# Kernel optimization log

Measured on AMD Instinct MI355X. Metric: run time of the kernel, lower is better.

The kernel has to match this reference:

```python
import jax, jax.numpy as jnp
import numpy as np

D_MODEL = 768
N_HEADS = 12
D_HEAD = 64
BATCH = 4
SEQ = 2048
INIT_RANGE = 0.02
IGNORE = -1e5


def setup_inputs() -> dict:
    key = jax.random.key(0)
    ks = jax.random.split(key, 5)
    x = jax.random.normal(ks[0], (BATCH, SEQ, D_MODEL), dtype=jnp.float32)
    W_Q = jax.random.normal(ks[1], (N_HEADS, D_MODEL, D_HEAD), dtype=jnp.float32) * INIT_RANGE
    W_K = jax.random.normal(ks[2], (N_HEADS, D_MODEL, D_HEAD), dtype=jnp.float32) * INIT_RANGE
    W_V = jax.random.normal(ks[3], (N_HEADS, D_MODEL, D_HEAD), dtype=jnp.float32) * INIT_RANGE
    W_O = jax.random.normal(ks[4], (N_HEADS, D_HEAD, D_MODEL), dtype=jnp.float32) * INIT_RANGE
    b_Q = jnp.zeros((N_HEADS, D_HEAD), dtype=jnp.float32)
    b_K = jnp.zeros((N_HEADS, D_HEAD), dtype=jnp.float32)
    b_V = jnp.zeros((N_HEADS, D_HEAD), dtype=jnp.float32)
    b_O = jnp.zeros((D_MODEL,), dtype=jnp.float32)
    return {"normalized_resid_pre": x, "W_Q": W_Q, "W_K": W_K, "W_V": W_V,
            "W_O": W_O, "b_Q": b_Q, "b_K": b_K, "b_V": b_V, "b_O": b_O}


def reference(normalized_resid_pre, W_Q, W_K, W_V, W_O, b_Q, b_K, b_V, b_O):
    x = normalized_resid_pre  # [b, s, d_model]
    q = jnp.einsum('bsm,hmd->bshd', x, W_Q) + b_Q  # [b, s, h, d_head]
    k = jnp.einsum('bsm,hmd->bshd', x, W_K) + b_K
    v = jnp.einsum('bsm,hmd->bshd', x, W_V) + b_V
    scores = jnp.einsum('bqhd,bkhd->bhqk', q, k) / jnp.sqrt(jnp.float32(D_HEAD))
    seq = x.shape[1]
    causal = jnp.tril(jnp.ones((seq, seq), dtype=bool))  # True where allowed
    scores = jnp.where(causal, scores, jnp.float32(IGNORE))
    pattern = jax.nn.softmax(scores, axis=-1)  # [b, h, q, k]
    z = jnp.einsum('bhqk,bkhd->bqhd', pattern, v)
    attn_out = jnp.einsum('bqhd,hdm->bqm', z, W_O) + b_O
    return attn_out
```

## Files before the change

### kernel.cpp

```cpp
#include <hip/hip_runtime.h>
#include <math.h>

#define DEVI __device__ __forceinline__

typedef __bf16 bf16_t;
typedef bf16_t bf16x8 __attribute__((ext_vector_type(8)));
typedef float  f32x4  __attribute__((ext_vector_type(4)));

constexpr int NB   = 4;
constexpr int SEQL = 2048;
constexpr int NH   = 12;
constexpr int DHD  = 64;
constexpr int DMOD = 768;
constexpr int NT   = NB * SEQL;
constexpr int KD   = DMOD;


DEVI unsigned short f2bf(float f) {
  union { float f; unsigned u; } v; v.f = f;
  unsigned r = v.u + 0x7FFFu + ((v.u >> 16) & 1u);
  return (unsigned short)(r >> 16);
}

DEVI unsigned short cvt_bf16(float f) {
  bf16_t b = (bf16_t)f;
  return __builtin_bit_cast(unsigned short, b);
}

DEVI float exp2_raw(float x) {
  float r;
  asm("v_exp_f32 %0, %1" : "=v"(r) : "v"(x));
  return r;
}

DEVI void gload16(const unsigned short* src, unsigned short* dst) {
  auto g = (const __attribute__((address_space(1))) unsigned int*)(unsigned long long)src;
  auto l = (__attribute__((address_space(3))) unsigned int*)(unsigned int)(unsigned long long)(dst);
  __builtin_amdgcn_global_load_lds(g, l, 16, 0, 0);
}

__global__ void __launch_bounds__(256) prep_all(const float* __restrict__ x,
                                                const float* __restrict__ WQ,
                                                const float* __restrict__ WK,
                                                const float* __restrict__ WV,
                                                const float* __restrict__ WO,
                                                unsigned short* __restrict__ xb,
                                                unsigned short* __restrict__ Wt,
                                                unsigned short* __restrict__ Wo_t) {
  __shared__ float T[64][68];
  const int bid = blockIdx.x;
  const int t = threadIdx.x;
  if (bid < 3072) {
    size_t i = ((size_t)bid * 256 + t) * 8;
    float4 a = *(const float4*)(x + i);
    float4 b = *(const float4*)(x + i + 4);
    union { unsigned short u[8]; uint4 v; } pk;
    pk.u[0] = f2bf(a.x); pk.u[1] = f2bf(a.y); pk.u[2] = f2bf(a.z); pk.u[3] = f2bf(a.w);
    pk.u[4] = f2bf(b.x); pk.u[5] = f2bf(b.y); pk.u[6] = f2bf(b.z); pk.u[7] = f2bf(b.w);
    *(uint4*)(xb + i) = pk.v;
    return;
  }
  const int r0 = t >> 4, c4 = (t & 15) * 4;
  if (bid < 3504) {
    const int u = bid - 3072;
    const int mt = u % 12, hw = u / 12;
    const int which = hw / 12, h = hw % 12;
    const float* W = (which == 0) ? WQ : ((which == 1) ? WK : WV);
    const float* src = W + ((size_t)h * 768 + mt * 64) * 64;
#pragma unroll
    for (int rep = 0; rep < 4; ++rep) {
      int m = rep * 16 + r0;
      float4 v = *(const float4*)(src + m * 64 + c4);
      T[m][c4] = v.x; T[m][c4 + 1] = v.y; T[m][c4 + 2] = v.z; T[m][c4 + 3] = v.w;
    }
    __syncthreads();
    unsigned short* dst = Wt + ((size_t)which * 768 + h * 64) * 768 + mt * 64;
#pragma unroll
    for (int rep = 0; rep < 4; ++rep) {
      int d = rep * 16 + r0;
      union { unsigned short u[4]; uint2 v; } o;
#pragma unroll
      for (int j = 0; j < 4; ++j) o.u[j] = f2bf(T[c4 + j][d]);
      *(uint2*)(dst + (size_t)d * 768 + c4) = o.v;
    }
  } else {
    const int u = bid - 3504;
    const int m0 = (u % 12) * 64, hd0 = (u / 12) * 64;
#pragma unroll
    for (int rep = 0; rep < 4; ++rep) {
      int i = rep * 16 + r0;
      float4 v = *(const float4*)(WO + (size_t)(hd0 + i) * 768 + m0 + c4);
      T[i][c4] = v.x; T[i][c4 + 1] = v.y; T[i][c4 + 2] = v.z; T[i][c4 + 3] = v.w;
    }
    __syncthreads();
#pragma unroll
    for (int rep = 0; rep < 4; ++rep) {
      int m = rep * 16 + r0;
      union { unsigned short u[4]; uint2 v; } o;
#pragma unroll
      for (int j = 0; j < 4; ++j) o.u[j] = f2bf(T[c4 + j][m]);
      *(uint2*)(Wo_t + (size_t)(m0 + m) * 768 + hd0 + c4) = o.v;
    }
  }
}

__global__ void __launch_bounds__(256)
gemm_qkv(const unsigned short* __restrict__ A,
         const unsigned short* __restrict__ Bt,
         const float* __restrict__ bq, const float* __restrict__ bk,
         const float* __restrict__ bv,
         unsigned short* __restrict__ qo, unsigned short* __restrict__ ko,
         unsigned short* __restrict__ vo) {
  __shared__ __align__(16) unsigned short ldsA[2 * 8192];
  __shared__ __align__(16) unsigned short ldsB[8192];
  const int bm = blockIdx.x, bn = blockIdx.y;
  const int m0 = bm * 128, n0 = bn * 128;
  const int tid = threadIdx.x, w = tid >> 6, lane = tid & 63;
  const int g = lane >> 4, r16 = lane & 15;
  const int wm = w >> 1, wn = w & 1;

  const int ss = (lane & 7) ^ ((lane >> 3) & 7);
  const unsigned short* asrc = A  + (size_t)(m0 + (lane >> 3)) * KD + ss * 8;
  const unsigned short* bsrc = Bt + (size_t)(n0 + (lane >> 3)) * KD + ss * 8;

  auto stageA = [&](int buf, int kt) {
#pragma unroll
    for (int j = 0; j < 4; ++j) {
      int seg = w * 4 + j;
      gload16(asrc + (size_t)(seg * 8) * KD + kt * 64, ldsA + buf * 8192 + seg * 512);
    }
  };
  auto stageB = [&](int kt) {
#pragma unroll
    for (int j = 0; j < 4; ++j) {
      int seg = w * 4 + j;
      gload16(bsrc + (size_t)(seg * 8) * KD + kt * 64, ldsB + seg * 512);
    }
  };

  const int r7 = r16 & 7;
  const int aoff0 = r16 * 64 + ((g    ) ^ r7) * 8;
  const int aoff1 = r16 * 64 + ((g + 4) ^ r7) * 8;

  f32x4 acc[4][4];
  const f32x4 zero4 = {0.f, 0.f, 0.f, 0.f};
#pragma unroll
  for (int i = 0; i < 4; ++i)
#pragma unroll
    for (int j = 0; j < 4; ++j) acc[i][j] = zero4;

  constexpr int NKT = KD / 64;
  stageA(0, 0);
  stageB(0);
  int buf = 0;
  for (int kt = 0; kt < NKT; ++kt) {
    if (kt + 1 < NKT) {
      stageA(buf ^ 1, kt + 1);
      asm volatile("s_waitcnt vmcnt(4)" ::: "memory");
    } else {
      asm volatile("s_waitcnt vmcnt(0)" ::: "memory");
    }
    __builtin_amdgcn_s_barrier();
    const unsigned short* Ab = ldsA + buf * 8192 + wm * 4096;
    const unsigned short* Bb = ldsB + wn * 4096;
    bf16x8 af[2][4], bfr[2][4];
#pragma unroll
    for (int f = 0; f < 4; ++f) {
      af[0][f]  = *(const bf16x8*)&Ab[aoff0 + f * 1024];
      af[1][f]  = *(const bf16x8*)&Ab[aoff1 + f * 1024];
      bfr[0][f] = *(const bf16x8*)&Bb[aoff0 + f * 1024];
      bfr[1][f] = *(const bf16x8*)&Bb[aoff1 + f * 1024];
    }
#pragma unroll
    for (int kk = 0; kk < 2; ++kk)
#pragma unroll
      for (int fm = 0; fm < 4; ++fm)
#pragma unroll
        for (int fn = 0; fn < 4; ++fn)
          acc[fm][fn] = __builtin_amdgcn_mfma_f32_16x16x32_bf16(af[kk][fm], bfr[kk][fn],
                                                                acc[fm][fn], 0, 0, 0);
    asm volatile("s_waitcnt lgkmcnt(0)" ::: "memory");
    __builtin_amdgcn_s_barrier();
    if (kt + 1 < NKT) stageB(kt + 1);
    buf ^= 1;
  }

#pragma unroll
  for (int fm = 0; fm < 4; ++fm) {
#pragma unroll
    for (int fn = 0; fn < 4; ++fn) {
      const int col = n0 + wn * 64 + fn * 16 + r16;
      const int rbase = m0 + wm * 64 + fm * 16 + g * 4;
      const int which = (col >= 1536) ? 2 : ((col >= 768) ? 1 : 0);
      const int hd = col - which * 768;
      const int h = hd >> 6, d = hd & 63;
      const float bias = (which == 0 ? bq : which == 1 ? bk : bv)[hd];
      if (which == 2) {
        union { unsigned short u[4]; uint2 v; } o;
#pragma unroll
        for (int r = 0; r < 4; ++r) o.u[r] = cvt_bf16(acc[fm][fn][r] + bias);
        const int b = rbase >> 11, s = rbase & (SEQL - 1);
        *(uint2*)(vo + ((size_t)(b * NH + h) * DHD + d) * SEQL + s) = o.v;
      } else {
#pragma unroll
        for (int r = 0; r < 4; ++r) {
          int row = rbase + r;
          int b = row >> 11, s = row & (SEQL - 1);
          float v = acc[fm][fn][r] + bias;
          if (which == 0)
            qo[((size_t)(b * NH + h) * SEQL + s) * DHD + d] = cvt_bf16(v * 0.1803368801111f);
          else
            ko[((size_t)(b * NH + h) * SEQL + s) * DHD + d] = cvt_bf16(v);
        }
      }
    }
  }
}

__global__ void __launch_bounds__(256)
gemm_o(const unsigned short* __restrict__ A,
       const unsigned short* __restrict__ Bt,
       const float* __restrict__ bo, float* __restrict__ fout) {
  __shared__ __align__(16) unsigned short ldsA[2 * 4096];
  __shared__ __align__(16) unsigned short ldsB[8192];
  const int bm = blockIdx.x, bn = blockIdx.y;
  const int m0 = bm * 64, n0 = bn * 128;
  const int tid = threadIdx.x, w = tid >> 6, lane = tid & 63;
  const int g = lane >> 4, r16 = lane & 15;
  const int wm = w >> 1, wn = w & 1;

  const int ss = (lane & 7) ^ ((lane >> 3) & 7);
  const unsigned short* asrc = A  + (size_t)(m0 + (lane >> 3)) * KD + ss * 8;
  const unsigned short* bsrc = Bt + (size_t)(n0 + (lane >> 3)) * KD + ss * 8;

  auto stageA = [&](int buf, int kt) {
#pragma unroll
    for (int j = 0; j < 2; ++j) {
      int seg = w * 2 + j;
      gload16(asrc + (size_t)(seg * 8) * KD + kt * 64, ldsA + buf * 4096 + seg * 512);
    }
  };
  auto stageB = [&](int kt) {
#pragma unroll
    for (int j = 0; j < 4; ++j) {
      int seg = w * 4 + j;
      gload16(bsrc + (size_t)(seg * 8) * KD + kt * 64, ldsB + seg * 512);
    }
  };

  const int r7 = r16 & 7;
  const int aoff0 = r16 * 64 + ((g    ) ^ r7) * 8;
  const int aoff1 = r16 * 64 + ((g + 4) ^ r7) * 8;

  f32x4 acc[2][4];
  const f32x4 zero4 = {0.f, 0.f, 0.f, 0.f};
#pragma unroll
  for (int i = 0; i < 2; ++i)
#pragma unroll
    for (int j = 0; j < 4; ++j) acc[i][j] = zero4;

  constexpr int NKT = KD / 64;
  stageA(0, 0);
  stageB(0);
  int buf = 0;
  for (int kt = 0; kt < NKT; ++kt) {
    if (kt + 1 < NKT) {
      stageA(buf ^ 1, kt + 1);
      asm volatile("s_waitcnt vmcnt(2)" ::: "memory");
    } else {
      asm volatile("s_waitcnt vmcnt(0)" ::: "memory");
    }
    __builtin_amdgcn_s_barrier();
    const unsigned short* Ab = ldsA + buf * 4096 + wm * 2048;
    const unsigned short* Bb = ldsB + wn * 4096;
    bf16x8 af[2][2], bfr[2][4];
#pragma unroll
    for (int f = 0; f < 2; ++f) {
      af[0][f] = *(const bf16x8*)&Ab[aoff0 + f * 1024];
      af[1][f] = *(const bf16x8*)&Ab[aoff1 + f * 1024];
    }
#pragma unroll
    for (int f = 0; f < 4; ++f) {
      bfr[0][f] = *(const bf16x8*)&Bb[aoff0 + f * 1024];
      bfr[1][f] = *(const bf16x8*)&Bb[aoff1 + f * 1024];
    }
#pragma unroll
    for (int kk = 0; kk < 2; ++kk)
#pragma unroll
      for (int fm = 0; fm < 2; ++fm)
#pragma unroll
        for (int fn = 0; fn < 4; ++fn)
          acc[fm][fn] = __builtin_amdgcn_mfma_f32_16x16x32_bf16(af[kk][fm], bfr[kk][fn],
                                                                acc[fm][fn], 0, 0, 0);
    asm volatile("s_waitcnt lgkmcnt(0)" ::: "memory");
    __builtin_amdgcn_s_barrier();
    if (kt + 1 < NKT) stageB(kt + 1);
    buf ^= 1;
  }

#pragma unroll
  for (int fm = 0; fm < 2; ++fm) {
#pragma unroll
    for (int fn = 0; fn < 4; ++fn) {
      const int col = n0 + wn * 64 + fn * 16 + r16;
      const int rbase = m0 + wm * 32 + fm * 16 + g * 4;
      const float bias = bo[col];
#pragma unroll
      for (int r = 0; r < 4; ++r)
        fout[(size_t)(rbase + r) * DMOD + col] = acc[fm][fn][r] + bias;
    }
  }
}

__global__ void __launch_bounds__(256, 3)
attn_fwd(const unsigned short* __restrict__ qb,
         const unsigned short* __restrict__ kb,
         const unsigned short* __restrict__ vt,
         unsigned short* __restrict__ zb) {
  __shared__ __align__(16) unsigned short ldsK[2 * 4096];
  __shared__ __align__(16) unsigned short ldsV[2 * 4096];
  __shared__ __align__(16) unsigned short ldsP[2 * 4096];
  const int id = blockIdx.x;
  const int qp = id / 48, bh = id % 48;
  const int qtA = qp, qtB = 31 - qp;
  const int tid = threadIdx.x, w = tid >> 6, lane = tid & 63;
  const int g = lane >> 4, r16 = lane & 15;
  const int r7 = r16 & 7;

  const int sslot = (lane & 7) ^ (lane >> 3);
  const unsigned short* ksrc = kb + (size_t)bh * SEQL * DHD + (lane >> 3) * 64 + sslot * 8;
  const unsigned short* vsrc = vt + (size_t)bh * SEQL * DHD + (lane >> 3) * 2048 + sslot * 8;

  auto stage = [&](int buf, int kv0) {
#pragma unroll
    for (int j = 0; j < 2; ++j) {
      int seg = w * 2 + j;
      gload16(ksrc + kv0 * 64 + seg * 512, ldsK + buf * 4096 + seg * 512);
      gload16(vsrc + kv0 + seg * 16384,    ldsV + buf * 4096 + seg * 512);
    }
  };

  const int roff0 = r16 * 64 + ((g    ) ^ r7) * 8;
  const int roff1 = r16 * 64 + ((g + 4) ^ r7) * 8;
  char* const pwbA = (char*)ldsP + w * 2048;
  char* const pwbB = (char*)ldsP + 8192 + w * 2048;
  int paddr[4];
#pragma unroll
  for (int fn = 0; fn < 4; ++fn)
    paddr[fn] = r16 * 128 + ((((fn * 2) + (g >> 1)) ^ r7) << 4) + ((g & 1) << 3);
  const int prd0 = r16 * 128 + (((g    ) ^ r7) << 4);
  const int prd1 = r16 * 128 + (((g + 4) ^ r7) << 4);
  const int thr = w * 16 + r16 - g * 4;

  bf16x8 qfA[2], qfB[2];
  {
    const unsigned short* qa = qb + ((size_t)bh * SEQL + qtA * 64 + w * 16 + r16) * DHD + g * 8;
    const unsigned short* qc = qb + ((size_t)bh * SEQL + qtB * 64 + w * 16 + r16) * DHD + g * 8;
    qfA[0] = *(const bf16x8*)qa; qfA[1] = *(const bf16x8*)(qa + 32);
    qfB[0] = *(const bf16x8*)qc; qfB[1] = *(const bf16x8*)(qc + 32);
  }

  float laccA = 0.f, laccB = 0.f;
  f32x4 zaccA[4], zaccB[4], saccA[4], saccB[4];
  const f32x4 zero4 = {0.f, 0.f, 0.f, 0.f};
#pragma unroll
  for (int r = 0; r < 4; ++r) { zaccA[r] = zero4; zaccB[r] = zero4; }

  auto qk = [&](const bf16x8* qf, f32x4* sacc, int buf) {
    const unsigned short* Kb = ldsK + buf * 4096;
    __builtin_amdgcn_s_setprio(1);
#pragma unroll
    for (int fn = 0; fn < 4; ++fn) {
      bf16x8 kf = *(const bf16x8*)&Kb[roff0 + fn * 1024];
      sacc[fn] = __builtin_amdgcn_mfma_f32_16x16x32_bf16(kf, qf[0], zero4, 0, 0, 0);
    }
#pragma unroll
    for (int fn = 0; fn < 4; ++fn) {
      bf16x8 kf = *(const bf16x8*)&Kb[roff1 + fn * 1024];
      sacc[fn] = __builtin_amdgcn_mfma_f32_16x16x32_bf16(kf, qf[1], sacc[fn], 0, 0, 0);
    }
    __builtin_amdgcn_s_setprio(0);
  };

  auto sm = [&](f32x4* sacc, float& lacc, char* pwb, bool diag) {
    if (diag) {
#pragma unroll
      for (int fn = 0; fn < 4; ++fn)
#pragma unroll
        for (int r = 0; r < 4; ++r)
          if (fn * 16 + r > thr) sacc[fn][r] = -3.0e38f;
    }
#pragma unroll
    for (int fn = 0; fn < 4; ++fn) {
      float p0 = exp2_raw(sacc[fn][0]), p1 = exp2_raw(sacc[fn][1]);
      float p2 = exp2_raw(sacc[fn][2]), p3 = exp2_raw(sacc[fn][3]);
      lacc += (p0 + p1) + (p2 + p3);
      unsigned w0, w1;
      asm("v_cvt_pk_bf16_f32 %0, %1, %2" : "=v"(w0) : "v"(p0), "v"(p1));
      asm("v_cvt_pk_bf16_f32 %0, %1, %2" : "=v"(w1) : "v"(p2), "v"(p3));
      uint2 pk; pk.x = w0; pk.y = w1;
      *(uint2*)(pwb + paddr[fn]) = pk;
    }
  };

  auto pv = [&](char* pwb, f32x4* zacc, int buf) {
    const unsigned short* Vb = ldsV + buf * 4096;
    bf16x8 pf0 = *(const bf16x8*)(pwb + prd0);
    bf16x8 pf1 = *(const bf16x8*)(pwb + prd1);
    __builtin_amdgcn_s_setprio(1);
#pragma unroll
    for (int fn = 0; fn < 4; ++fn) {
      bf16x8 vf = *(const bf16x8*)&Vb[roff0 + fn * 1024];
      zacc[fn] = __builtin_amdgcn_mfma_f32_16x16x32_bf16(pf0, vf, zacc[fn], 0, 0, 0);
    }
#pragma unroll
    for (int fn = 0; fn < 4; ++fn) {
      bf16x8 vf = *(const bf16x8*)&Vb[roff1 + fn * 1024];
      zacc[fn] = __builtin_amdgcn_mfma_f32_16x16x32_bf16(pf1, vf, zacc[fn], 0, 0, 0);
    }
    __builtin_amdgcn_s_setprio(0);
  };

  stage(0, 0);
  asm volatile("s_waitcnt vmcnt(0)" ::: "memory");
  __builtin_amdgcn_s_barrier();

  int buf = 0;
  for (int kt = 0; kt <= qtB; ++kt) {
    if (kt) __builtin_amdgcn_s_barrier();
    if (kt < qtB) {
      stage(buf ^ 1, (kt + 1) * 64);
      if (kt) asm volatile("s_waitcnt vmcnt(4)" ::: "memory");
    } else {
      asm volatile("s_waitcnt vmcnt(0)" ::: "memory");
    }
    const bool doA = (kt <= qtA);
    qk(qfB, saccB, buf);
    if (doA) qk(qfA, saccA, buf);
    sm(saccB, laccB, pwbB, kt == qtB);
    if (doA) sm(saccA, laccA, pwbA, kt == qtA);
    asm volatile("" ::: "memory");
    pv(pwbB, zaccB, buf);
    if (doA) pv(pwbA, zaccA, buf);
    buf ^= 1;
  }

  laccA += __shfl_xor(laccA, 16); laccA += __shfl_xor(laccA, 32);
  laccB += __shfl_xor(laccB, 16); laccB += __shfl_xor(laccB, 32);
  const float invA = 1.0f / laccA;
  const float invB = 1.0f / laccB;
  const int b = bh / NH, h = bh % NH;
#pragma unroll
  for (int r = 0; r < 4; ++r) {
    float iar = __shfl(invA, g * 4 + r);
    float ibr = __shfl(invB, g * 4 + r);
    int sA = qtA * 64 + w * 16 + g * 4 + r;
    int sB = qtB * 64 + w * 16 + g * 4 + r;
#pragma unroll
    for (int fn = 0; fn < 4; ++fn) {
      int d = fn * 16 + r16;
      zb[((size_t)(b * SEQL + sA)) * DMOD + h * DHD + d] = cvt_bf16(zaccA[fn][r] * iar);
      zb[((size_t)(b * SEQL + sB)) * DMOD + h * DHD + d] = cvt_bf16(zaccB[fn][r] * ibr);
    }
  }
}


extern "C" void kernel_launch(void* const* d_in, const int* in_sizes, int n_in,
                              void* d_out, int out_size, void* d_ws, size_t ws_size,
                              hipStream_t stream) {
  const float* x  = (const float*)d_in[0];
  const float* WQ = (const float*)d_in[1];
  const float* WK = (const float*)d_in[2];
  const float* WV = (const float*)d_in[3];
  const float* WO = (const float*)d_in[4];
  const float* bQ = (const float*)d_in[5];
  const float* bK = (const float*)d_in[6];
  const float* bV = (const float*)d_in[7];
  const float* bO = (const float*)d_in[8];
  float* out = (float*)d_out;

  constexpr size_t NE = (size_t)NT * DMOD;
  unsigned short* w0   = (unsigned short*)d_ws;
  unsigned short* Wqkv = w0;
  unsigned short* Wo   = Wqkv + (size_t)3 * 768 * 768;
  unsigned short* xb   = Wo + (size_t)768 * 768;
  unsigned short* qb   = xb + NE;
  unsigned short* kb   = qb + NE;
  unsigned short* vt   = kb + NE;
  unsigned short* zb   = xb;
  size_t need = (size_t)(vt + NE - w0) * sizeof(unsigned short);
  if (ws_size < need) return;

  prep_all<<<3648, 256, 0, stream>>>(x, WQ, WK, WV, WO, xb, Wqkv, Wo);
  gemm_qkv<<<dim3(64, 18), 256, 0, stream>>>(xb, Wqkv, bQ, bK, bV, qb, kb, vt);
  attn_fwd<<<768, 256, 0, stream>>>(qb, kb, vt, zb);
  gemm_o<<<dim3(128, 6), 256, 0, stream>>>(zb, Wo, bO, out);
}
```

Measured before the change: 106.0 us.

## Software-pipeline QK and PV across iterations, pass P via bpermute

Restructures the attention loop so the PV matmul for the previous KV tile is issued alongside the QK matmul of the current tile, with softmax moved after it. V gets a triple-buffered LDS ring to support the one-tile lag. The P tile now moves between lanes in registers with ds_bpermute instead of an LDS write/read round trip, and the row sums come from an MFMA against a ones vector instead of scalar adds and shuffles. This is meant to overlap exp/convert work with matrix work and drop the P LDS traffic, at the cost of more registers, extra LDS for V, and row sums taken from bf16-rounded P.

```diff
diff --git a/kernel.cpp b/kernel.cpp
--- a/kernel.cpp
+++ b/kernel.cpp
@@ -312,14 +312,15 @@
   }
 }
 
+struct PS { unsigned s[4][2]; };
+
 __global__ void __launch_bounds__(256, 3)
 attn_fwd(const unsigned short* __restrict__ qb,
          const unsigned short* __restrict__ kb,
          const unsigned short* __restrict__ vt,
          unsigned short* __restrict__ zb) {
   __shared__ __align__(16) unsigned short ldsK[2 * 4096];
-  __shared__ __align__(16) unsigned short ldsV[2 * 4096];
-  __shared__ __align__(16) unsigned short ldsP[2 * 4096];
+  __shared__ __align__(16) unsigned short ldsV[3 * 4096];
   const int id = blockIdx.x;
   const int qp = id / 48, bh = id % 48;
   const int qtA = qp, qtB = 31 - qp;
@@ -331,26 +332,22 @@
   const unsigned short* ksrc = kb + (size_t)bh * SEQL * DHD + (lane >> 3) * 64 + sslot * 8;
   const unsigned short* vsrc = vt + (size_t)bh * SEQL * DHD + (lane >> 3) * 2048 + sslot * 8;
 
-  auto stage = [&](int buf, int kv0) {
+  auto stage = [&](int kslot, int vslot, int kv0) {
 #pragma unroll
     for (int j = 0; j < 2; ++j) {
       int seg = w * 2 + j;
-      gload16(ksrc + kv0 * 64 + seg * 512, ldsK + buf * 4096 + seg * 512);
-      gload16(vsrc + kv0 + seg * 16384,    ldsV + buf * 4096 + seg * 512);
+      gload16(ksrc + kv0 * 64 + seg * 512, ldsK + kslot * 4096 + seg * 512);
+      gload16(vsrc + kv0 + seg * 16384,    ldsV + vslot * 4096 + seg * 512);
     }
   };
 
   const int roff0 = r16 * 64 + ((g    ) ^ r7) * 8;
   const int roff1 = r16 * 64 + ((g + 4) ^ r7) * 8;
-  char* const pwbA = (char*)ldsP + w * 2048;
-  char* const pwbB = (char*)ldsP + 8192 + w * 2048;
-  int paddr[4];
-#pragma unroll
-  for (int fn = 0; fn < 4; ++fn)
-    paddr[fn] = r16 * 128 + ((((fn * 2) + (g >> 1)) ^ r7) << 4) + ((g & 1) << 3);
-  const int prd0 = r16 * 128 + (((g    ) ^ r7) << 4);
-  const int prd1 = r16 * 128 + (((g + 4) ^ r7) << 4);
   const int thr = w * 16 + r16 - g * 4;
+
+  const int bpa0 = ((((lane >> 4) & 1) << 5) + r16) << 2;
+  const int bpa1 = bpa0 + 64;
+  const bool glow = (lane < 32);
 
   bf16x8 qfA[2], qfB[2];
   {
@@ -360,15 +357,18 @@
     qfB[0] = *(const bf16x8*)qc; qfB[1] = *(const bf16x8*)(qc + 32);
   }
 
-  float laccA = 0.f, laccB = 0.f;
+  const bf16_t one1 = (bf16_t)1.0f;
+  const bf16x8 ones = {one1, one1, one1, one1, one1, one1, one1, one1};
+
   f32x4 zaccA[4], zaccB[4], saccA[4], saccB[4];
+  f32x4 lsumA, lsumB;
   const f32x4 zero4 = {0.f, 0.f, 0.f, 0.f};
 #pragma unroll
   for (int r = 0; r < 4; ++r) { zaccA[r] = zero4; zaccB[r] = zero4; }
-
-  auto qk = [&](const bf16x8* qf, f32x4* sacc, int buf) {
-    const unsigned short* Kb = ldsK + buf * 4096;
-    __builtin_amdgcn_s_setprio(1);
+  lsumA = zero4; lsumB = zero4;
+
+  auto qk = [&](const bf16x8* qf, f32x4* sacc, int kslot) {
+    const unsigned short* Kb = ldsK + kslot * 4096;
 #pragma unroll
     for (int fn = 0; fn < 4; ++fn) {
       bf16x8 kf = *(const bf16x8*)&Kb[roff0 + fn * 1024];
@@ -379,10 +379,9 @@
       bf16x8 kf = *(const bf16x8*)&Kb[roff1 + fn * 1024];
       sacc[fn] = __builtin_amdgcn_mfma_f32_16x16x32_bf16(kf, qf[1], sacc[fn], 0, 0, 0);
     }
-    __builtin_amdgcn_s_setprio(0);
-  };
-
-  auto sm = [&](f32x4* sacc, float& lacc, char* pwb, bool diag) {
+  };
+
+  auto sm = [&](f32x4* sacc, PS& S, bool diag) {
     if (diag) {
 #pragma unroll
       for (int fn = 0; fn < 4; ++fn)
@@ -394,66 +393,82 @@
     for (int fn = 0; fn < 4; ++fn) {
       float p0 = exp2_raw(sacc[fn][0]), p1 = exp2_raw(sacc[fn][1]);
       float p2 = exp2_raw(sacc[fn][2]), p3 = exp2_raw(sacc[fn][3]);
-      lacc += (p0 + p1) + (p2 + p3);
-      unsigned w0, w1;
-      asm("v_cvt_pk_bf16_f32 %0, %1, %2" : "=v"(w0) : "v"(p0), "v"(p1));
-      asm("v_cvt_pk_bf16_f32 %0, %1, %2" : "=v"(w1) : "v"(p2), "v"(p3));
-      uint2 pk; pk.x = w0; pk.y = w1;
-      *(uint2*)(pwb + paddr[fn]) = pk;
-    }
-  };
-
-  auto pv = [&](char* pwb, f32x4* zacc, int buf) {
-    const unsigned short* Vb = ldsV + buf * 4096;
-    bf16x8 pf0 = *(const bf16x8*)(pwb + prd0);
-    bf16x8 pf1 = *(const bf16x8*)(pwb + prd1);
-    __builtin_amdgcn_s_setprio(1);
+      asm("v_cvt_pk_bf16_f32 %0, %1, %2" : "=v"(S.s[fn][0]) : "v"(p0), "v"(p1));
+      asm("v_cvt_pk_bf16_f32 %0, %1, %2" : "=v"(S.s[fn][1]) : "v"(p2), "v"(p3));
+    }
+  };
+
+  auto pv = [&](const PS& S, f32x4* zacc, f32x4& lsum, int vslot) {
+    const unsigned short* Vb = ldsV + vslot * 4096;
+    int a0 = __builtin_amdgcn_ds_bpermute(bpa0, (int)S.s[0][0]);
+    int a1 = __builtin_amdgcn_ds_bpermute(bpa0, (int)S.s[0][1]);
+    int a2 = __builtin_amdgcn_ds_bpermute(bpa1, (int)S.s[0][0]);
+    int a3 = __builtin_amdgcn_ds_bpermute(bpa1, (int)S.s[0][1]);
+    int b0 = __builtin_amdgcn_ds_bpermute(bpa0, (int)S.s[1][0]);
+    int b1 = __builtin_amdgcn_ds_bpermute(bpa0, (int)S.s[1][1]);
+    int b2 = __builtin_amdgcn_ds_bpermute(bpa1, (int)S.s[1][0]);
+    int b3 = __builtin_amdgcn_ds_bpermute(bpa1, (int)S.s[1][1]);
+    int c0 = __builtin_amdgcn_ds_bpermute(bpa0, (int)S.s[2][0]);
+    int c1 = __builtin_amdgcn_ds_bpermute(bpa0, (int)S.s[2][1]);
+    int c2 = __builtin_amdgcn_ds_bpermute(bpa1, (int)S.s[2][0]);
+    int c3 = __builtin_amdgcn_ds_bpermute(bpa1, (int)S.s[2][1]);
+    int d0 = __builtin_amdgcn_ds_bpermute(bpa0, (int)S.s[3][0]);
+    int d1 = __builtin_amdgcn_ds_bpermute(bpa0, (int)S.s[3][1]);
+    int d2 = __builtin_amdgcn_ds_bpermute(bpa1, (int)S.s[3][0]);
+    int d3 = __builtin_amdgcn_ds_bpermute(bpa1, (int)S.s[3][1]);
+    uint4 t0, t1;
+    t0.x = (unsigned)(glow ? a0 : b0); t0.y = (unsigned)(glow ? a1 : b1);
+    t0.z = (unsigned)(glow ? a2 : b2); t0.w = (unsigned)(glow ? a3 : b3);
+    t1.x = (unsigned)(glow ? c0 : d0); t1.y = (unsigned)(glow ? c1 : d1);
+    t1.z = (unsigned)(glow ? c2 : d2); t1.w = (unsigned)(glow ? c3 : d3);
+    bf16x8 pf0 = __builtin_bit_cast(bf16x8, t0);
+    bf16x8 pf1 = __builtin_bit_cast(bf16x8, t1);
 #pragma unroll
     for (int fn = 0; fn < 4; ++fn) {
       bf16x8 vf = *(const bf16x8*)&Vb[roff0 + fn * 1024];
       zacc[fn] = __builtin_amdgcn_mfma_f32_16x16x32_bf16(pf0, vf, zacc[fn], 0, 0, 0);
     }
+    lsum = __builtin_amdgcn_mfma_f32_16x16x32_bf16(pf0, ones, lsum, 0, 0, 0);
 #pragma unroll
     for (int fn = 0; fn < 4; ++fn) {
       bf16x8 vf = *(const bf16x8*)&Vb[roff1 + fn * 1024];
       zacc[fn] = __builtin_amdgcn_mfma_f32_16x16x32_bf16(pf1, vf, zacc[fn], 0, 0, 0);
     }
-    __builtin_amdgcn_s_setprio(0);
-  };
-
-  stage(0, 0);
+    lsum = __builtin_amdgcn_mfma_f32_16x16x32_bf16(pf1, ones, lsum, 0, 0, 0);
+  };
+
+  stage(0, 0, 0);
   asm volatile("s_waitcnt vmcnt(0)" ::: "memory");
   __builtin_amdgcn_s_barrier();
 
-  int buf = 0;
+  PS SA, SB;
   for (int kt = 0; kt <= qtB; ++kt) {
     if (kt) __builtin_amdgcn_s_barrier();
     if (kt < qtB) {
-      stage(buf ^ 1, (kt + 1) * 64);
-      if (kt) asm volatile("s_waitcnt vmcnt(4)" ::: "memory");
+      stage((kt + 1) & 1, (kt + 1) % 3, (kt + 1) * 64);
+      asm volatile("s_waitcnt vmcnt(4)" ::: "memory");
     } else {
       asm volatile("s_waitcnt vmcnt(0)" ::: "memory");
     }
     const bool doA = (kt <= qtA);
-    qk(qfB, saccB, buf);
-    if (doA) qk(qfA, saccA, buf);
-    sm(saccB, laccB, pwbB, kt == qtB);
-    if (doA) sm(saccA, laccA, pwbA, kt == qtA);
-    asm volatile("" ::: "memory");
-    pv(pwbB, zaccB, buf);
-    if (doA) pv(pwbA, zaccA, buf);
-    buf ^= 1;
-  }
-
-  laccA += __shfl_xor(laccA, 16); laccA += __shfl_xor(laccA, 32);
-  laccB += __shfl_xor(laccB, 16); laccB += __shfl_xor(laccB, 32);
-  const float invA = 1.0f / laccA;
-  const float invB = 1.0f / laccB;
+    __builtin_amdgcn_s_setprio(1);
+    qk(qfB, saccB, kt & 1);
+    if (doA) qk(qfA, saccA, kt & 1);
+    if (kt) {
+      pv(SB, zaccB, lsumB, (kt - 1) % 3);
+      if (kt - 1 <= qtA) pv(SA, zaccA, lsumA, (kt - 1) % 3);
+    }
+    __builtin_amdgcn_s_setprio(0);
+    sm(saccB, SB, kt == qtB);
+    if (doA) sm(saccA, SA, kt == qtA);
+  }
+  pv(SB, zaccB, lsumB, qtB % 3);
+
   const int b = bh / NH, h = bh % NH;
 #pragma unroll
   for (int r = 0; r < 4; ++r) {
-    float iar = __shfl(invA, g * 4 + r);
-    float ibr = __shfl(invB, g * 4 + r);
+    float iar = 1.0f / lsumA[r];
+    float ibr = 1.0f / lsumB[r];
     int sA = qtA * 64 + w * 16 + g * 4 + r;
     int sB = qtB * 64 + w * 16 + g * 4 + r;
 #pragma unroll
```

Measured after the change: 111.5 us. +5.2%, slower.

## Rewrite attention kernel with 32x32 MFMA tiles and adjacent query-tile pairing

Applied to the files above, without the earlier changes.

Changes the attention kernel from 16x16x32 MFMA fragments to 32x32x16 MFMA, with each wave owning 32 query rows across two adjacent query tiles instead of a front/back tile pair per block. Row sums are now computed by an extra MFMA against a ones vector rather than scalar adds and shuffles, and block-to-tile mapping alternates low/high tile pairs for causal load balance. The aim is higher MFMA efficiency and fewer VALU/shuffle ops. The cost is imbalance inside a block, since waves on the lower tile sit idle on the last iteration, plus an extra MFMA per step for the sums.

```diff
diff --git a/kernel.cpp b/kernel.cpp
--- a/kernel.cpp
+++ b/kernel.cpp
@@ -6,6 +6,7 @@
 typedef __bf16 bf16_t;
 typedef bf16_t bf16x8 __attribute__((ext_vector_type(8)));
 typedef float  f32x4  __attribute__((ext_vector_type(4)));
+typedef float  f32x16 __attribute__((ext_vector_type(16)));
 
 constexpr int NB   = 4;
 constexpr int SEQL = 2048;
@@ -319,13 +320,16 @@
          unsigned short* __restrict__ zb) {
   __shared__ __align__(16) unsigned short ldsK[2 * 4096];
   __shared__ __align__(16) unsigned short ldsV[2 * 4096];
-  __shared__ __align__(16) unsigned short ldsP[2 * 4096];
+  __shared__ __align__(16) unsigned short ldsP[4 * 2048];
   const int id = blockIdx.x;
-  const int qp = id / 48, bh = id % 48;
-  const int qtA = qp, qtB = 31 - qp;
+  const int kap = id / 48, bh = id % 48;
+  const int k2 = (kap & 1) ? (15 - (kap >> 1)) : (kap >> 1);
+  const int qt1 = 2 * k2 + 1;
   const int tid = threadIdx.x, w = tid >> 6, lane = tid & 63;
-  const int g = lane >> 4, r16 = lane & 15;
-  const int r7 = r16 & 7;
+  const int l31 = lane & 31, hi = lane >> 5, l7 = lane & 7;
+  const int myqt = 2 * k2 + (w >> 1);
+  const int qrow = myqt * 64 + (w & 1) * 32;
+  const int thr = (w & 1) * 32 + l31;
 
   const int sslot = (lane & 7) ^ (lane >> 3);
   const unsigned short* ksrc = kb + (size_t)bh * SEQL * DHD + (lane >> 3) * 64 + sslot * 8;
@@ -340,128 +344,98 @@
     }
   };
 
-  const int roff0 = r16 * 64 + ((g    ) ^ r7) * 8;
-  const int roff1 = r16 * 64 + ((g + 4) ^ r7) * 8;
-  char* const pwbA = (char*)ldsP + w * 2048;
-  char* const pwbB = (char*)ldsP + 8192 + w * 2048;
-  int paddr[4];
-#pragma unroll
-  for (int fn = 0; fn < 4; ++fn)
-    paddr[fn] = r16 * 128 + ((((fn * 2) + (g >> 1)) ^ r7) << 4) + ((g & 1) << 3);
-  const int prd0 = r16 * 128 + (((g    ) ^ r7) << 4);
-  const int prd1 = r16 * 128 + (((g + 4) ^ r7) << 4);
-  const int thr = w * 16 + r16 - g * 4;
-
-  bf16x8 qfA[2], qfB[2];
+  bf16x8 qf[4];
   {
-    const unsigned short* qa = qb + ((size_t)bh * SEQL + qtA * 64 + w * 16 + r16) * DHD + g * 8;
-    const unsigned short* qc = qb + ((size_t)bh * SEQL + qtB * 64 + w * 16 + r16) * DHD + g * 8;
-    qfA[0] = *(const bf16x8*)qa; qfA[1] = *(const bf16x8*)(qa + 32);
-    qfB[0] = *(const bf16x8*)qc; qfB[1] = *(const bf16x8*)(qc + 32);
-  }
-
-  float laccA = 0.f, laccB = 0.f;
-  f32x4 zaccA[4], zaccB[4], saccA[4], saccB[4];
-  const f32x4 zero4 = {0.f, 0.f, 0.f, 0.f};
-#pragma unroll
-  for (int r = 0; r < 4; ++r) { zaccA[r] = zero4; zaccB[r] = zero4; }
-
-  auto qk = [&](const bf16x8* qf, f32x4* sacc, int buf) {
-    const unsigned short* Kb = ldsK + buf * 4096;
-    __builtin_amdgcn_s_setprio(1);
-#pragma unroll
-    for (int fn = 0; fn < 4; ++fn) {
-      bf16x8 kf = *(const bf16x8*)&Kb[roff0 + fn * 1024];
-      sacc[fn] = __builtin_amdgcn_mfma_f32_16x16x32_bf16(kf, qf[0], zero4, 0, 0, 0);
-    }
-#pragma unroll
-    for (int fn = 0; fn < 4; ++fn) {
-      bf16x8 kf = *(const bf16x8*)&Kb[roff1 + fn * 1024];
-      sacc[fn] = __builtin_amdgcn_mfma_f32_16x16x32_bf16(kf, qf[1], sacc[fn], 0, 0, 0);
-    }
-    __builtin_amdgcn_s_setprio(0);
-  };
-
-  auto sm = [&](f32x4* sacc, float& lacc, char* pwb, bool diag) {
-    if (diag) {
-#pragma unroll
-      for (int fn = 0; fn < 4; ++fn)
-#pragma unroll
-        for (int r = 0; r < 4; ++r)
-          if (fn * 16 + r > thr) sacc[fn][r] = -3.0e38f;
-    }
-#pragma unroll
-    for (int fn = 0; fn < 4; ++fn) {
-      float p0 = exp2_raw(sacc[fn][0]), p1 = exp2_raw(sacc[fn][1]);
-      float p2 = exp2_raw(sacc[fn][2]), p3 = exp2_raw(sacc[fn][3]);
-      lacc += (p0 + p1) + (p2 + p3);
-      unsigned w0, w1;
-      asm("v_cvt_pk_bf16_f32 %0, %1, %2" : "=v"(w0) : "v"(p0), "v"(p1));
-      asm("v_cvt_pk_bf16_f32 %0, %1, %2" : "=v"(w1) : "v"(p2), "v"(p3));
-      uint2 pk; pk.x = w0; pk.y = w1;
-      *(uint2*)(pwb + paddr[fn]) = pk;
-    }
-  };
-
-  auto pv = [&](char* pwb, f32x4* zacc, int buf) {
-    const unsigned short* Vb = ldsV + buf * 4096;
-    bf16x8 pf0 = *(const bf16x8*)(pwb + prd0);
-    bf16x8 pf1 = *(const bf16x8*)(pwb + prd1);
-    __builtin_amdgcn_s_setprio(1);
-#pragma unroll
-    for (int fn = 0; fn < 4; ++fn) {
-      bf16x8 vf = *(const bf16x8*)&Vb[roff0 + fn * 1024];
-      zacc[fn] = __builtin_amdgcn_mfma_f32_16x16x32_bf16(pf0, vf, zacc[fn], 0, 0, 0);
-    }
-#pragma unroll
-    for (int fn = 0; fn < 4; ++fn) {
-      bf16x8 vf = *(const bf16x8*)&Vb[roff1 + fn * 1024];
-      zacc[fn] = __builtin_amdgcn_mfma_f32_16x16x32_bf16(pf1, vf, zacc[fn], 0, 0, 0);
-    }
-    __builtin_amdgcn_s_setprio(0);
-  };
+    const unsigned short* qp = qb + ((size_t)bh * SEQL + qrow + l31) * DHD + hi * 8;
+#pragma unroll
+    for (int ks = 0; ks < 4; ++ks) qf[ks] = *(const bf16x8*)(qp + ks * 16);
+  }
+
+  const bf16_t one1 = (bf16_t)1.0f;
+  const bf16x8 onesB = {one1, one1, one1, one1, one1, one1, one1, one1};
+  f32x16 zacc0, zacc1, lsum;
+  const f32x16 zero16 = {0.f, 0.f, 0.f, 0.f, 0.f, 0.f, 0.f, 0.f,
+                         0.f, 0.f, 0.f, 0.f, 0.f, 0.f, 0.f, 0.f};
+  zacc0 = zero16; zacc1 = zero16; lsum = zero16;
+
+  unsigned short* const pwb = ldsP + w * 2048;
 
   stage(0, 0);
   asm volatile("s_waitcnt vmcnt(0)" ::: "memory");
   __builtin_amdgcn_s_barrier();
 
-  int buf = 0;
-  for (int kt = 0; kt <= qtB; ++kt) {
+  for (int kt = 0; kt <= qt1; ++kt) {
     if (kt) __builtin_amdgcn_s_barrier();
-    if (kt < qtB) {
-      stage(buf ^ 1, (kt + 1) * 64);
+    if (kt < qt1) {
+      stage((kt + 1) & 1, (kt + 1) * 64);
       if (kt) asm volatile("s_waitcnt vmcnt(4)" ::: "memory");
     } else {
       asm volatile("s_waitcnt vmcnt(0)" ::: "memory");
     }
-    const bool doA = (kt <= qtA);
-    qk(qfB, saccB, buf);
-    if (doA) qk(qfA, saccA, buf);
-    sm(saccB, laccB, pwbB, kt == qtB);
-    if (doA) sm(saccA, laccA, pwbA, kt == qtA);
-    asm volatile("" ::: "memory");
-    pv(pwbB, zaccB, buf);
-    if (doA) pv(pwbA, zaccA, buf);
-    buf ^= 1;
-  }
-
-  laccA += __shfl_xor(laccA, 16); laccA += __shfl_xor(laccA, 32);
-  laccB += __shfl_xor(laccB, 16); laccB += __shfl_xor(laccB, 32);
-  const float invA = 1.0f / laccA;
-  const float invB = 1.0f / laccB;
+    if (kt <= myqt) {
+      const unsigned short* Kb = ldsK + (kt & 1) * 4096;
+      const unsigned short* Vb = ldsV + (kt & 1) * 4096;
+      const bool diag = (kt == myqt);
+      f32x16 s0 = zero16, s1 = zero16;
+      __builtin_amdgcn_s_setprio(1);
+#pragma unroll
+      for (int ks = 0; ks < 4; ++ks) {
+        const int c = ((2 * ks + hi) ^ l7) * 8;
+        bf16x8 kf0 = *(const bf16x8*)&Kb[l31 * 64 + c];
+        bf16x8 kf1 = *(const bf16x8*)&Kb[(32 + l31) * 64 + c];
+        s0 = __builtin_amdgcn_mfma_f32_32x32x16_bf16(kf0, qf[ks], s0, 0, 0, 0);
+        s1 = __builtin_amdgcn_mfma_f32_32x32x16_bf16(kf1, qf[ks], s1, 0, 0, 0);
+      }
+      __builtin_amdgcn_s_setprio(0);
+#pragma unroll
+      for (int fn = 0; fn < 2; ++fn) {
+        f32x16 s = fn ? s1 : s0;
+        if (diag) {
+#pragma unroll
+          for (int r = 0; r < 16; ++r) {
+            int kv = 32 * fn + (r & 3) + 8 * (r >> 2) + 4 * hi;
+            if (kv > thr) s[r] = -3.0e38f;
+          }
+        }
+        float p[16];
+#pragma unroll
+        for (int r = 0; r < 16; ++r) p[r] = exp2_raw(s[r]);
+#pragma unroll
+        for (int rq = 0; rq < 4; ++rq) {
+          unsigned d0, d1;
+          asm("v_cvt_pk_bf16_f32 %0, %1, %2" : "=v"(d0) : "v"(p[4*rq]),   "v"(p[4*rq+1]));
+          asm("v_cvt_pk_bf16_f32 %0, %1, %2" : "=v"(d1) : "v"(p[4*rq+2]), "v"(p[4*rq+3]));
+          uint2 pk2; pk2.x = d0; pk2.y = d1;
+          *(uint2*)((char*)pwb + l31 * 128 + (((4 * fn + rq) ^ l7) << 4) + hi * 8) = pk2;
+        }
+      }
+      asm volatile("" ::: "memory");
+      bf16x8 pf[4];
+#pragma unroll
+      for (int m = 0; m < 4; ++m)
+        pf[m] = *(const bf16x8*)&pwb[l31 * 64 + (((2 * m + hi) ^ l7) << 3)];
+      __builtin_amdgcn_s_setprio(1);
+#pragma unroll
+      for (int m = 0; m < 4; ++m) {
+        const int c = ((2 * m + hi) ^ l7) * 8;
+        bf16x8 vf0 = *(const bf16x8*)&Vb[l31 * 64 + c];
+        bf16x8 vf1 = *(const bf16x8*)&Vb[(32 + l31) * 64 + c];
+        zacc0 = __builtin_amdgcn_mfma_f32_32x32x16_bf16(pf[m], vf0, zacc0, 0, 0, 0);
+        zacc1 = __builtin_amdgcn_mfma_f32_32x32x16_bf16(pf[m], vf1, zacc1, 0, 0, 0);
+        lsum  = __builtin_amdgcn_mfma_f32_32x32x16_bf16(pf[m], onesB, lsum, 0, 0, 0);
+      }
+      __builtin_amdgcn_s_setprio(0);
+    }
+  }
+
   const int b = bh / NH, h = bh % NH;
 #pragma unroll
-  for (int r = 0; r < 4; ++r) {
-    float iar = __shfl(invA, g * 4 + r);
-    float ibr = __shfl(invB, g * 4 + r);
-    int sA = qtA * 64 + w * 16 + g * 4 + r;
-    int sB = qtB * 64 + w * 16 + g * 4 + r;
-#pragma unroll
-    for (int fn = 0; fn < 4; ++fn) {
-      int d = fn * 16 + r16;
-      zb[((size_t)(b * SEQL + sA)) * DMOD + h * DHD + d] = cvt_bf16(zaccA[fn][r] * iar);
-      zb[((size_t)(b * SEQL + sB)) * DMOD + h * DHD + d] = cvt_bf16(zaccB[fn][r] * ibr);
-    }
+  for (int r = 0; r < 16; ++r) {
+    float inv = 1.0f / lsum[r];
+    int q = qrow + (r & 3) + 8 * (r >> 2) + 4 * hi;
+    size_t base = ((size_t)(b * SEQL + q)) * DMOD + h * DHD;
+    zb[base + l31]      = cvt_bf16(zacc0[r] * inv);
+    zb[base + 32 + l31] = cvt_bf16(zacc1[r] * inv);
   }
 }
 
```

Result: slower. 112.2 us (+5.8%).

## Software-pipeline PV of previous tile with QK of current tile; MFMA row sums

Applied to the files above, without the earlier changes.

Restructures the attention main loop so the P·V product for the previous key tile is issued right after the Q·K product for the current tile, with softmax exp moved after a barrier and overlapping the next tile's global load. QK and PV for the two query tiles are interleaved so each K/V fragment loaded from LDS feeds both. Softmax row sums now come from extra MFMAs against a ones vector instead of scalar adds and cross-lane shuffles. The row sum is now taken from bf16-rounded probabilities, and the barrier and wait pattern changes (full vmcnt(0) wait each iteration), which could expose load latency.

```diff
diff --git a/kernel.cpp b/kernel.cpp
--- a/kernel.cpp
+++ b/kernel.cpp
@@ -360,29 +360,16 @@
     qfB[0] = *(const bf16x8*)qc; qfB[1] = *(const bf16x8*)(qc + 32);
   }
 
-  float laccA = 0.f, laccB = 0.f;
-  f32x4 zaccA[4], zaccB[4], saccA[4], saccB[4];
+  const bf16_t one1 = (bf16_t)1.0f;
+  const bf16x8 ones = {one1, one1, one1, one1, one1, one1, one1, one1};
+
+  f32x4 zaccA[4], zaccB[4], saccA[4], saccB[4], lsumA, lsumB;
   const f32x4 zero4 = {0.f, 0.f, 0.f, 0.f};
 #pragma unroll
   for (int r = 0; r < 4; ++r) { zaccA[r] = zero4; zaccB[r] = zero4; }
-
-  auto qk = [&](const bf16x8* qf, f32x4* sacc, int buf) {
-    const unsigned short* Kb = ldsK + buf * 4096;
-    __builtin_amdgcn_s_setprio(1);
-#pragma unroll
-    for (int fn = 0; fn < 4; ++fn) {
-      bf16x8 kf = *(const bf16x8*)&Kb[roff0 + fn * 1024];
-      sacc[fn] = __builtin_amdgcn_mfma_f32_16x16x32_bf16(kf, qf[0], zero4, 0, 0, 0);
-    }
-#pragma unroll
-    for (int fn = 0; fn < 4; ++fn) {
-      bf16x8 kf = *(const bf16x8*)&Kb[roff1 + fn * 1024];
-      sacc[fn] = __builtin_amdgcn_mfma_f32_16x16x32_bf16(kf, qf[1], sacc[fn], 0, 0, 0);
-    }
-    __builtin_amdgcn_s_setprio(0);
-  };
-
-  auto sm = [&](f32x4* sacc, float& lacc, char* pwb, bool diag) {
+  lsumA = zero4; lsumB = zero4;
+
+  auto sm = [&](f32x4* sacc, char* pwb, bool diag) {
     if (diag) {
 #pragma unroll
       for (int fn = 0; fn < 4; ++fn)
@@ -394,7 +381,6 @@
     for (int fn = 0; fn < 4; ++fn) {
       float p0 = exp2_raw(sacc[fn][0]), p1 = exp2_raw(sacc[fn][1]);
       float p2 = exp2_raw(sacc[fn][2]), p3 = exp2_raw(sacc[fn][3]);
-      lacc += (p0 + p1) + (p2 + p3);
       unsigned w0, w1;
       asm("v_cvt_pk_bf16_f32 %0, %1, %2" : "=v"(w0) : "v"(p0), "v"(p1));
       asm("v_cvt_pk_bf16_f32 %0, %1, %2" : "=v"(w1) : "v"(p2), "v"(p3));
@@ -403,57 +389,84 @@
     }
   };
 
-  auto pv = [&](char* pwb, f32x4* zacc, int buf) {
-    const unsigned short* Vb = ldsV + buf * 4096;
-    bf16x8 pf0 = *(const bf16x8*)(pwb + prd0);
-    bf16x8 pf1 = *(const bf16x8*)(pwb + prd1);
+  auto pv2 = [&](bool do2, const unsigned short* Vb) {
+    bf16x8 pB0 = *(const bf16x8*)(pwbB + prd0);
+    bf16x8 pB1 = *(const bf16x8*)(pwbB + prd1);
+    bf16x8 pA0, pA1;
+    if (do2) { pA0 = *(const bf16x8*)(pwbA + prd0); pA1 = *(const bf16x8*)(pwbA + prd1); }
+#pragma unroll
+    for (int fn = 0; fn < 4; ++fn) {
+      bf16x8 vf = *(const bf16x8*)&Vb[roff0 + fn * 1024];
+      zaccB[fn] = __builtin_amdgcn_mfma_f32_16x16x32_bf16(pB0, vf, zaccB[fn], 0, 0, 0);
+      if (do2) zaccA[fn] = __builtin_amdgcn_mfma_f32_16x16x32_bf16(pA0, vf, zaccA[fn], 0, 0, 0);
+    }
+    lsumB = __builtin_amdgcn_mfma_f32_16x16x32_bf16(pB0, ones, lsumB, 0, 0, 0);
+    if (do2) lsumA = __builtin_amdgcn_mfma_f32_16x16x32_bf16(pA0, ones, lsumA, 0, 0, 0);
+#pragma unroll
+    for (int fn = 0; fn < 4; ++fn) {
+      bf16x8 vf = *(const bf16x8*)&Vb[roff1 + fn * 1024];
+      zaccB[fn] = __builtin_amdgcn_mfma_f32_16x16x32_bf16(pB1, vf, zaccB[fn], 0, 0, 0);
+      if (do2) zaccA[fn] = __builtin_amdgcn_mfma_f32_16x16x32_bf16(pA1, vf, zaccA[fn], 0, 0, 0);
+    }
+    lsumB = __builtin_amdgcn_mfma_f32_16x16x32_bf16(pB1, ones, lsumB, 0, 0, 0);
+    if (do2) lsumA = __builtin_amdgcn_mfma_f32_16x16x32_bf16(pA1, ones, lsumA, 0, 0, 0);
+  };
+
+  stage(0, 0);
+
+  for (int kt = 0; kt <= qtB; ++kt) {
+    __builtin_amdgcn_s_barrier();
+    asm volatile("s_waitcnt vmcnt(0)" ::: "memory");
+    const bool doA = (kt <= qtA);
+    const unsigned short* Kb = ldsK + (kt & 1) * 4096;
     __builtin_amdgcn_s_setprio(1);
 #pragma unroll
     for (int fn = 0; fn < 4; ++fn) {
+      bf16x8 kf = *(const bf16x8*)&Kb[roff0 + fn * 1024];
+      saccB[fn] = __builtin_amdgcn_mfma_f32_16x16x32_bf16(kf, qfB[0], zero4, 0, 0, 0);
+      if (doA) saccA[fn] = __builtin_amdgcn_mfma_f32_16x16x32_bf16(kf, qfA[0], zero4, 0, 0, 0);
+    }
+#pragma unroll
+    for (int fn = 0; fn < 4; ++fn) {
+      bf16x8 kf = *(const bf16x8*)&Kb[roff1 + fn * 1024];
+      saccB[fn] = __builtin_amdgcn_mfma_f32_16x16x32_bf16(kf, qfB[1], saccB[fn], 0, 0, 0);
+      if (doA) saccA[fn] = __builtin_amdgcn_mfma_f32_16x16x32_bf16(kf, qfA[1], saccA[fn], 0, 0, 0);
+    }
+    if (kt) {
+      asm volatile("" ::: "memory");
+      pv2(kt - 1 <= qtA, ldsV + ((kt - 1) & 1) * 4096);
+    }
+    __builtin_amdgcn_s_setprio(0);
+    __builtin_amdgcn_s_barrier();
+    if (kt < qtB) stage((kt + 1) & 1, (kt + 1) * 64);
+    sm(saccB, pwbB, kt == qtB);
+    if (doA) sm(saccA, pwbA, kt == qtA);
+  }
+
+  asm volatile("" ::: "memory");
+  {
+    const unsigned short* Vb = ldsV + (qtB & 1) * 4096;
+    bf16x8 pB0 = *(const bf16x8*)(pwbB + prd0);
+    bf16x8 pB1 = *(const bf16x8*)(pwbB + prd1);
+#pragma unroll
+    for (int fn = 0; fn < 4; ++fn) {
       bf16x8 vf = *(const bf16x8*)&Vb[roff0 + fn * 1024];
-      zacc[fn] = __builtin_amdgcn_mfma_f32_16x16x32_bf16(pf0, vf, zacc[fn], 0, 0, 0);
-    }
+      zaccB[fn] = __builtin_amdgcn_mfma_f32_16x16x32_bf16(pB0, vf, zaccB[fn], 0, 0, 0);
+    }
+    lsumB = __builtin_amdgcn_mfma_f32_16x16x32_bf16(pB0, ones, lsumB, 0, 0, 0);
 #pragma unroll
     for (int fn = 0; fn < 4; ++fn) {
       bf16x8 vf = *(const bf16x8*)&Vb[roff1 + fn * 1024];
-      zacc[fn] = __builtin_amdgcn_mfma_f32_16x16x32_bf16(pf1, vf, zacc[fn], 0, 0, 0);
-    }
-    __builtin_amdgcn_s_setprio(0);
-  };
-
-  stage(0, 0);
-  asm volatile("s_waitcnt vmcnt(0)" ::: "memory");
-  __builtin_amdgcn_s_barrier();
-
-  int buf = 0;
-  for (int kt = 0; kt <= qtB; ++kt) {
-    if (kt) __builtin_amdgcn_s_barrier();
-    if (kt < qtB) {
-      stage(buf ^ 1, (kt + 1) * 64);
-      if (kt) asm volatile("s_waitcnt vmcnt(4)" ::: "memory");
-    } else {
-      asm volatile("s_waitcnt vmcnt(0)" ::: "memory");
-    }
-    const bool doA = (kt <= qtA);
-    qk(qfB, saccB, buf);
-    if (doA) qk(qfA, saccA, buf);
-    sm(saccB, laccB, pwbB, kt == qtB);
-    if (doA) sm(saccA, laccA, pwbA, kt == qtA);
-    asm volatile("" ::: "memory");
-    pv(pwbB, zaccB, buf);
-    if (doA) pv(pwbA, zaccA, buf);
-    buf ^= 1;
-  }
-
-  laccA += __shfl_xor(laccA, 16); laccA += __shfl_xor(laccA, 32);
-  laccB += __shfl_xor(laccB, 16); laccB += __shfl_xor(laccB, 32);
-  const float invA = 1.0f / laccA;
-  const float invB = 1.0f / laccB;
+      zaccB[fn] = __builtin_amdgcn_mfma_f32_16x16x32_bf16(pB1, vf, zaccB[fn], 0, 0, 0);
+    }
+    lsumB = __builtin_amdgcn_mfma_f32_16x16x32_bf16(pB1, ones, lsumB, 0, 0, 0);
+  }
+
   const int b = bh / NH, h = bh % NH;
 #pragma unroll
   for (int r = 0; r < 4; ++r) {
-    float iar = __shfl(invA, g * 4 + r);
-    float ibr = __shfl(invB, g * 4 + r);
+    float iar = 1.0f / lsumA[r];
+    float ibr = 1.0f / lsumB[r];
     int sA = qtA * 64 + w * 16 + g * 4 + r;
     int sB = qtB * 64 + w * 16 + g * 4 + r;
 #pragma unroll
```

Result: slower. 113.6 us (+7.1%).
